# Performance work log

Measured on AMD Instinct MI355X. Metric: run time of the kernel, lower is better.

The kernel has to match this reference:

```python
import jax, jax.numpy as jnp
import numpy as np

N_TYPES = 4  # global / and / or / leaf node types (indep_weights)


def gcn_layer(x, W_stack, b, edge_src, edge_dst, edge_w, labels, num_nodes):
    # Per-node-type dense projection: compute all 4 projections, then select by label.
    # all4: [4, N, out]
    all4 = jnp.einsum('nd,kdo->kno', x, W_stack)
    support = jnp.take_along_axis(all4, labels[None, :, None].astype(jnp.int32), axis=0)[0]  # [N, out]
    # Sparse adjacency propagation: out[dst] += w * support[src]  (torch.spmm equivalent)
    msgs = support[edge_src] * edge_w[:, None]  # [E, out]
    agg = jax.ops.segment_sum(msgs, edge_dst, num_segments=num_nodes)
    return agg + b


def setup_inputs() -> dict:
    key = jax.random.key(0)
    ks = jax.random.split(key, 12)
    N, E = 50000, 1600000
    nfeat, nhid, nclass = 256, 256, 64
    x = jax.random.normal(ks[0], (N, nfeat), dtype=jnp.float32)
    edge_src = jax.random.randint(ks[1], (E,), 0, N, dtype=jnp.int32)
    edge_dst = jax.random.randint(ks[2], (E,), 0, N, dtype=jnp.int32)
    edge_w = jax.random.uniform(ks[3], (E,), dtype=jnp.float32)
    labels = jax.random.randint(ks[4], (N,), 0, N_TYPES, dtype=jnp.int32)
    def winit(k, fi, fo):
        s = 1.0 / np.sqrt(fo)
        return jax.random.uniform(k, (N_TYPES, fi, fo), minval=-s, maxval=s, dtype=jnp.float32)
    def binit(k, fo):
        s = 1.0 / np.sqrt(fo)
        return jax.random.uniform(k, (fo,), minval=-s, maxval=s, dtype=jnp.float32)
    return {
        'x': x, 'edge_src': edge_src, 'edge_dst': edge_dst, 'edge_w': edge_w, 'labels': labels,
        'W1': winit(ks[5], nfeat, nhid), 'b1': binit(ks[6], nhid),
        'W2': winit(ks[7], nhid, nhid), 'b2': binit(ks[8], nhid),
        'W3': winit(ks[9], nhid, nclass), 'b3': binit(ks[10], nclass),
    }


def reference(x, edge_src, edge_dst, edge_w, labels, W1, b1, W2, b2, W3, b3):
    N = x.shape[0]
    h = jax.nn.relu(gcn_layer(x, W1, b1, edge_src, edge_dst, edge_w, labels, N))
    # F.dropout with p=0 (module default) is identity
    h = jax.nn.relu(gcn_layer(h, W2, b2, edge_src, edge_dst, edge_w, labels, N))
    out = gcn_layer(h, W3, b3, edge_src, edge_dst, edge_w, labels, N)
    return out
```

## Files before the change

kernel.cpp:

```cpp
#include <hip/hip_runtime.h>
#include <hip/hip_bf16.h>

#define NT 4
#define FEAT 256
#define OUT3 64

typedef __bf16 bf16x8 __attribute__((ext_vector_type(8)));
typedef float  f32x4  __attribute__((ext_vector_type(4)));

__device__ inline unsigned int f2bf_bits(float f) {
    __hip_bfloat16 h = __float2bfloat16(f);
    unsigned short u;
    __builtin_memcpy(&u, &h, 2);
    return (unsigned int)u;
}
__device__ inline float bfl(unsigned int u) { return __uint_as_float(u << 16); }
__device__ inline float bfh(unsigned int u) { return __uint_as_float(u & 0xffff0000u); }

__global__ void zero_small(int* __restrict__ bcnt, int* __restrict__ lc, int* __restrict__ lcur) {
    int i = threadIdx.x;
    bcnt[i] = 0;
    if (i < NT) { lc[i] = 0; lcur[i] = 0; }
}

__global__ __launch_bounds__(512) void bucket_count(const int* __restrict__ dst,
                                                    const int* __restrict__ labels,
                                                    int* __restrict__ bcnt, int* __restrict__ lc,
                                                    int E, int N) {
    __shared__ int h[256];
    __shared__ int lh[NT];
    int tid = threadIdx.x;
    if (tid < 256) h[tid] = 0;
    if (tid < NT) lh[tid] = 0;
    __syncthreads();
    int base = blockIdx.x * 4096;
#pragma unroll
    for (int k = 0; k < 8; ++k) {
        int e = base + k * 512 + tid;
        if (e < E) atomicAdd(&h[((unsigned)dst[e]) >> 8], 1);
    }
#pragma unroll
    for (int k = 0; k < 8; ++k) {
        int i = base + k * 512 + tid;
        if (i < N) atomicAdd(&lh[labels[i]], 1);
    }
    __syncthreads();
    if (tid < 256) { int v = h[tid]; if (v) atomicAdd(&bcnt[tid], v); }
    if (tid < NT) { int v = lh[tid]; if (v) atomicAdd(&lc[tid], v); }
}

__global__ __launch_bounds__(256) void scan_master(
    const int* __restrict__ bcnt, const int* __restrict__ lc,
    int* __restrict__ boff, int* __restrict__ gcur, int* __restrict__ rowoff,
    int* __restrict__ lstart, int* __restrict__ perm,
    int NB, int N, int E, int permCap) {
    __shared__ int s[256];
    int tid = threadIdx.x;
    int own = (tid < NB) ? bcnt[tid] : 0;
    s[tid] = own;
    __syncthreads();
    for (int d = 1; d < 256; d <<= 1) {
        int v = (tid >= d) ? s[tid - d] : 0;
        __syncthreads();
        s[tid] += v;
        __syncthreads();
    }
    int excl = s[tid] - own;
    if (tid < NB) { boff[tid] = excl; gcur[tid] = excl; }
    if (tid == 0) {
        boff[NB] = E; rowoff[N] = E;
        int run = 0;
        int ls[NT], cnt[NT];
        for (int l = 0; l < NT; ++l) {
            ls[l] = run; cnt[l] = lc[l];
            lstart[l] = run;
            run += (cnt[l] + 63) & ~63;
        }
        for (int l = 0; l < NT; ++l) {
            int end = (l + 1 < NT) ? ls[l + 1] : run;
            for (int i = ls[l] + cnt[l]; i < end; ++i) perm[i] = -1;
        }
        for (int i = run; i < permCap; ++i) perm[i] = -1;
    }
}

__global__ __launch_bounds__(512) void scatter_combined(
    const int* __restrict__ src, const int* __restrict__ dst, const float* __restrict__ w,
    int* __restrict__ gcur, uint2* __restrict__ earr, int E, int nbEB,
    const int* __restrict__ labels, const int* __restrict__ lstart,
    int* __restrict__ lcur, int* __restrict__ perm, int N) {
    int tid = threadIdx.x;
    if ((int)blockIdx.x < nbEB) {
        __shared__ int h[256];
        __shared__ int basearr[256];
        if (tid < 256) h[tid] = 0;
        __syncthreads();
        int base = blockIdx.x * 4096;
        int b[8], rank[8], px[8]; float wv[8];
#pragma unroll
        for (int k = 0; k < 8; ++k) {
            int e = base + k * 512 + tid;
            if (e < E) {
                int d = dst[e];
                b[k] = ((unsigned)d) >> 8;
                px[k] = src[e] | ((d & 255) << 16);
                wv[k] = w[e];
                rank[k] = atomicAdd(&h[b[k]], 1);
            } else b[k] = -1;
        }
        __syncthreads();
        if (tid < 256) { int c = h[tid]; basearr[tid] = c ? atomicAdd(&gcur[tid], c) : 0; }
        __syncthreads();
#pragma unroll
        for (int k = 0; k < 8; ++k) {
            if (b[k] >= 0) {
                int pos = basearr[b[k]] + rank[k];
                earr[pos] = make_uint2((unsigned)px[k], __float_as_uint(wv[k]));
            }
        }
    } else {
        int n = ((int)blockIdx.x - nbEB) * 512 + tid;
        int lab = (n < N) ? labels[n] : -1;
        int lane = tid & 63;
        for (int l = 0; l < NT; ++l) {
            unsigned long long m = __ballot(lab == l);
            if (m == 0ull) continue;
            int leader = __builtin_ctzll(m);
            int base = 0;
            if (lane == leader) base = atomicAdd(&lcur[l], (int)__popcll(m));
            base = __shfl(base, leader, 64);
            if (lab == l) {
                int prefix = (int)__popcll(m & ((1ull << lane) - 1ull));
                perm[lstart[l] + base + prefix] = n;
            }
        }
    }
}

__global__ __launch_bounds__(1024) void bucket_sort(
    const uint2* __restrict__ earr, const int* __restrict__ boff,
    int* __restrict__ rowoff, unsigned int* __restrict__ edata, int N) {
    int b = blockIdx.x;
    int s = boff[b], e = boff[b + 1];
    __shared__ int cnt[256], off[256];
    int tid = threadIdx.x;
    if (tid < 256) cnt[tid] = 0;
    __syncthreads();
    for (int i = s + tid; i < e; i += 1024) atomicAdd(&cnt[(earr[i].x >> 16) & 255], 1);
    __syncthreads();
    if (tid < 256) off[tid] = cnt[tid];
    __syncthreads();
    for (int d = 1; d < 256; d <<= 1) {
        int v = 0;
        if (tid < 256 && tid >= d) v = off[tid - d];
        __syncthreads();
        if (tid < 256) off[tid] += v;
        __syncthreads();
    }
    if (tid < 256) {
        int excl = off[tid] - cnt[tid];
        int node = b * 256 + tid;
        if (node < N) rowoff[node] = s + excl;
        off[tid] = excl;
    }
    __syncthreads();
    for (int i = s + tid; i < e; i += 1024) {
        uint2 r = earr[i];
        int d = (r.x >> 16) & 255;
        int k = atomicAdd(&off[d], 1);
        edata[s + k] = (f2bf_bits(__uint_as_float(r.y)) << 16) | (r.x & 0xffff);
    }
}

__global__ void cast_x(const float* __restrict__ x, unsigned short* __restrict__ xb, int total4) {
    int i = blockIdx.x * 256 + threadIdx.x;
    if (i < total4) {
        const float4* xv = (const float4*)x;
        float4 v = xv[i];
        unsigned int lo = f2bf_bits(v.x) | (f2bf_bits(v.y) << 16);
        unsigned int hi = f2bf_bits(v.z) | (f2bf_bits(v.w) << 16);
        uint2 o; o.x = lo; o.y = hi;
        ((uint2*)xb)[i] = o;
    }
}

__global__ void cast_w_all(const float* __restrict__ W1, const float* __restrict__ W2,
                           const float* __restrict__ W3, unsigned short* __restrict__ W1b,
                           unsigned short* __restrict__ W2b, unsigned short* __restrict__ W3b) {
    const int S = NT * FEAT * FEAT;
    int idx = blockIdx.x * 256 + threadIdx.x;
    const float* W; unsigned short* D; int OUTF; int t;
    if (idx < S)            { W = W1; D = W1b; OUTF = FEAT; t = idx; }
    else if (idx < 2 * S)   { W = W2; D = W2b; OUTF = FEAT; t = idx - S; }
    else if (idx < 2 * S + NT * FEAT * OUT3) { W = W3; D = W3b; OUTF = OUT3; t = idx - 2 * S; }
    else return;
    int n = t % OUTF;
    int r = t / OUTF;
    int j = r & 7, q = (r >> 3) & 3, k0 = (r >> 5) & 7, lab = r >> 8;
    int k = k0 * 32 + q * 8 + j;
    float f = W[((size_t)(lab * FEAT + k)) * OUTF + n];
    D[(((size_t)lab * 8 + k0) * OUTF + n) * 32 + q * 8 + j] = (unsigned short)f2bf_bits(f);
}

__global__ __launch_bounds__(256) void proj256_kernel(
    const unsigned short* __restrict__ xb, const unsigned short* __restrict__ Wswz,
    const int* __restrict__ perm, const int* __restrict__ labels,
    unsigned short* __restrict__ outp) {
    int warp = threadIdx.x >> 6;
    int lane = threadIdx.x & 63;
    int m0 = blockIdx.x * 64;
    int first = perm[m0];
    if (first < 0) return;
    int lab = labels[first];
    int q = lane >> 4, c = lane & 15;
    int n0 = warp * 64;

    const unsigned short* arow[4];
#pragma unroll
    for (int t = 0; t < 4; ++t) {
        int nd = perm[m0 + t * 16 + c];
        arow[t] = xb + (size_t)((nd < 0) ? first : nd) * FEAT;
    }
    const unsigned short* bb = Wswz + (size_t)lab * FEAT * 256 + (size_t)(n0 + c) * 32 + q * 8;

    f32x4 acc[4][4] = {};
#pragma unroll
    for (int k0 = 0; k0 < 8; ++k0) {
        bf16x8 a[4];
#pragma unroll
        for (int t = 0; t < 4; ++t) a[t] = *(const bf16x8*)(arow[t] + k0 * 32 + q * 8);
        const unsigned short* bk = bb + (size_t)k0 * 32 * 256;
#pragma unroll
        for (int u = 0; u < 4; ++u) {
            bf16x8 bfrag = *(const bf16x8*)(bk + u * 512);
#pragma unroll
            for (int t = 0; t < 4; ++t)
                acc[t][u] = __builtin_amdgcn_mfma_f32_16x16x32_bf16(a[t], bfrag, acc[t][u], 0, 0, 0);
        }
    }
    __hip_bfloat16* ob = (__hip_bfloat16*)outp;
#pragma unroll
    for (int t = 0; t < 4; ++t) {
#pragma unroll
        for (int r = 0; r < 4; ++r) {
            int noder = perm[m0 + t * 16 + q * 4 + r];
            if (noder >= 0) {
#pragma unroll
                for (int u = 0; u < 4; ++u)
                    ob[(size_t)noder * 256 + n0 + u * 16 + c] = __float2bfloat16(acc[t][u][r]);
            }
        }
    }
}

__global__ __launch_bounds__(256) void proj64_kernel(
    const unsigned short* __restrict__ xb, const unsigned short* __restrict__ Wswz,
    const int* __restrict__ perm, const int* __restrict__ labels,
    unsigned short* __restrict__ outp) {
    int warp = threadIdx.x >> 6;
    int lane = threadIdx.x & 63;
    int m0 = blockIdx.x * 64;
    int first = perm[m0];
    if (first < 0) return;
    int lab = labels[first];
    int q = lane >> 4, c = lane & 15;
    int mb = m0 + warp * 16;

    int ndc = perm[mb + c];
    const unsigned short* arow = xb + (size_t)((ndc < 0) ? first : ndc) * FEAT;
    const unsigned short* bb = Wswz + (size_t)lab * FEAT * OUT3 + (size_t)c * 32 + q * 8;

    f32x4 acc[4] = {};
#pragma unroll
    for (int k0 = 0; k0 < 8; ++k0) {
        bf16x8 a = *(const bf16x8*)(arow + k0 * 32 + q * 8);
        const unsigned short* bk = bb + (size_t)k0 * 32 * OUT3;
#pragma unroll
        for (int u = 0; u < 4; ++u) {
            bf16x8 bfrag = *(const bf16x8*)(bk + u * 512);
            acc[u] = __builtin_amdgcn_mfma_f32_16x16x32_bf16(a, bfrag, acc[u], 0, 0, 0);
        }
    }
    __hip_bfloat16* ob = (__hip_bfloat16*)outp;
#pragma unroll
    for (int r = 0; r < 4; ++r) {
        int noder = perm[mb + q * 4 + r];
        if (noder >= 0) {
#pragma unroll
            for (int u = 0; u < 4; ++u)
                ob[(size_t)noder * OUT3 + u * 16 + c] = __float2bfloat16(acc[u][r]);
        }
    }
}

__global__ __launch_bounds__(256) void agg256_kernel(
    const uint2* __restrict__ sup, const int* __restrict__ rowoff,
    const unsigned int* __restrict__ edata, const float* __restrict__ bias,
    uint2* __restrict__ outp, int N) {
    int warp = __builtin_amdgcn_readfirstlane((int)(threadIdx.x >> 6));
    int node = (int)blockIdx.x * 4 + warp;
    if (node >= N) return;
    int lane = threadIdx.x & 63;
    int s = __builtin_amdgcn_readfirstlane(rowoff[node]);
    int e = __builtin_amdgcn_readfirstlane(rowoff[node + 1]);
    float a0 = 0.f, a1 = 0.f, a2 = 0.f, a3 = 0.f;
    int j = s;
    for (; j + 8 <= e; j += 8) {
        int ed[8]; uint2 v[8];
#pragma unroll
        for (int u = 0; u < 8; ++u) ed[u] = __builtin_amdgcn_readfirstlane((int)edata[j + u]);
#pragma unroll
        for (int u = 0; u < 8; ++u) v[u] = sup[(size_t)(ed[u] & 0xffff) * 64 + lane];
#pragma unroll
        for (int u = 0; u < 8; ++u) {
            float w = __uint_as_float((unsigned int)ed[u] & 0xffff0000u);
            a0 += w * bfl(v[u].x); a1 += w * bfh(v[u].x);
            a2 += w * bfl(v[u].y); a3 += w * bfh(v[u].y);
        }
    }
    if (j < e) {
        int ed[8]; float wm[8]; uint2 v[8];
#pragma unroll
        for (int u = 0; u < 8; ++u) {
            int jj = j + u;
            int jc = (jj < e) ? jj : e - 1;
            ed[u] = __builtin_amdgcn_readfirstlane((int)edata[jc]);
            wm[u] = (jj < e) ? __uint_as_float((unsigned int)ed[u] & 0xffff0000u) : 0.f;
        }
#pragma unroll
        for (int u = 0; u < 8; ++u) v[u] = sup[(size_t)(ed[u] & 0xffff) * 64 + lane];
#pragma unroll
        for (int u = 0; u < 8; ++u) {
            a0 += wm[u] * bfl(v[u].x); a1 += wm[u] * bfh(v[u].x);
            a2 += wm[u] * bfl(v[u].y); a3 += wm[u] * bfh(v[u].y);
        }
    }
    float4 b = ((const float4*)bias)[lane];
    a0 = fmaxf(a0 + b.x, 0.f);
    a1 = fmaxf(a1 + b.y, 0.f);
    a2 = fmaxf(a2 + b.z, 0.f);
    a3 = fmaxf(a3 + b.w, 0.f);
    unsigned int lo = f2bf_bits(a0) | (f2bf_bits(a1) << 16);
    unsigned int hi = f2bf_bits(a2) | (f2bf_bits(a3) << 16);
    outp[(size_t)node * 64 + lane] = make_uint2(lo, hi);
}

__global__ __launch_bounds__(256) void agg64_kernel(
    const unsigned short* __restrict__ sup, const int* __restrict__ rowoff,
    const unsigned int* __restrict__ edata, const float* __restrict__ bias,
    float* __restrict__ outp, int N) {
    int warp = __builtin_amdgcn_readfirstlane((int)(threadIdx.x >> 6));
    int node = (int)blockIdx.x * 4 + warp;
    if (node >= N) return;
    int lane = threadIdx.x & 63;
    int s = __builtin_amdgcn_readfirstlane(rowoff[node]);
    int e = __builtin_amdgcn_readfirstlane(rowoff[node + 1]);
    float a = 0.f;
    int j = s;
    for (; j + 8 <= e; j += 8) {
        int ed[8]; unsigned short v[8];
#pragma unroll
        for (int u = 0; u < 8; ++u) ed[u] = __builtin_amdgcn_readfirstlane((int)edata[j + u]);
#pragma unroll
        for (int u = 0; u < 8; ++u) v[u] = sup[(size_t)(ed[u] & 0xffff) * 64 + lane];
#pragma unroll
        for (int u = 0; u < 8; ++u)
            a += __uint_as_float((unsigned int)ed[u] & 0xffff0000u) * __uint_as_float((unsigned int)v[u] << 16);
    }
    if (j < e) {
        int ed[8]; float wm[8]; unsigned short v[8];
#pragma unroll
        for (int u = 0; u < 8; ++u) {
            int jj = j + u;
            int jc = (jj < e) ? jj : e - 1;
            ed[u] = __builtin_amdgcn_readfirstlane((int)edata[jc]);
            wm[u] = (jj < e) ? __uint_as_float((unsigned int)ed[u] & 0xffff0000u) : 0.f;
        }
#pragma unroll
        for (int u = 0; u < 8; ++u) v[u] = sup[(size_t)(ed[u] & 0xffff) * 64 + lane];
#pragma unroll
        for (int u = 0; u < 8; ++u)
            a += wm[u] * __uint_as_float((unsigned int)v[u] << 16);
    }
    a += bias[lane];
    outp[(size_t)node * 64 + lane] = a;
}

extern "C" void kernel_launch(void* const* d_in, const int* in_sizes, int n_in,
                              void* d_out, int out_size, void* d_ws, size_t ws_size,
                              hipStream_t stream) {
    const float* x        = (const float*)d_in[0];
    const int*   edge_src = (const int*)d_in[1];
    const int*   edge_dst = (const int*)d_in[2];
    const float* edge_w   = (const float*)d_in[3];
    const int*   labels   = (const int*)d_in[4];
    const float* W1 = (const float*)d_in[5];
    const float* b1 = (const float*)d_in[6];
    const float* W2 = (const float*)d_in[7];
    const float* b2 = (const float*)d_in[8];
    const float* W3 = (const float*)d_in[9];
    const float* b3 = (const float*)d_in[10];

    const int N = in_sizes[0] / FEAT;
    const int E = in_sizes[1];
    const int NB = (N + 255) >> 8;
    const int G64 = (N + NT * 64 + 63) / 64;
    const int permCap = G64 * 64;

    char* p = (char*)d_ws;
    auto alloc = [&](size_t bytes) -> char* {
        char* r = p;
        p += (bytes + 255) & ~(size_t)255;
        return r;
    };
    unsigned short* bufA = (unsigned short*)alloc((size_t)N * FEAT * 2);
    unsigned short* bufB = (unsigned short*)alloc((size_t)N * FEAT * 2);
    unsigned short* W1b  = (unsigned short*)alloc((size_t)NT * FEAT * FEAT * 2);
    unsigned short* W2b  = (unsigned short*)alloc((size_t)NT * FEAT * FEAT * 2);
    unsigned short* W3b  = (unsigned short*)alloc((size_t)NT * FEAT * OUT3 * 2);
    int*          rowoff = (int*)alloc((size_t)(N + 1) * 4);
    unsigned int* edata  = (unsigned int*)alloc((size_t)E * 4);
    int*          perm   = (int*)alloc((size_t)permCap * 4);
    int*          bcnt   = (int*)alloc(256 * 4);
    int*          boff   = (int*)alloc(257 * 4);
    int*          gcur   = (int*)alloc(256 * 4);
    int*          lc     = (int*)alloc(64);
    int*          lcur   = (int*)alloc(64);
    int*          lstart = (int*)alloc(64);
    uint2* earr = (uint2*)bufA;

    const int nbEB = (E + 4095) / 4096;
    const int nbN  = (N + 511) / 512;

    zero_small<<<1, 256, 0, stream>>>(bcnt, lc, lcur);
    bucket_count<<<nbEB, 512, 0, stream>>>(edge_dst, labels, bcnt, lc, E, N);
    scan_master<<<1, 256, 0, stream>>>(bcnt, lc, boff, gcur, rowoff, lstart, perm, NB, N, E, permCap);
    scatter_combined<<<nbEB + nbN, 512, 0, stream>>>(edge_src, edge_dst, edge_w, gcur, earr, E, nbEB,
                                                     labels, lstart, lcur, perm, N);
    bucket_sort<<<NB, 1024, 0, stream>>>(earr, boff, rowoff, edata, N);

    cast_x<<<((N * FEAT / 4) + 255) / 256, 256, 0, stream>>>(x, bufA, N * FEAT / 4);
    {
        int totalW = 2 * NT * FEAT * FEAT + NT * FEAT * OUT3;
        cast_w_all<<<(totalW + 255) / 256, 256, 0, stream>>>(W1, W2, W3, W1b, W2b, W3b);
    }

    proj256_kernel<<<G64, 256, 0, stream>>>(bufA, W1b, perm, labels, bufB);
    agg256_kernel<<<(N + 3) / 4, 256, 0, stream>>>((const uint2*)bufB, rowoff, edata, b1, (uint2*)bufA, N);
    proj256_kernel<<<G64, 256, 0, stream>>>(bufA, W2b, perm, labels, bufB);
    agg256_kernel<<<(N + 3) / 4, 256, 0, stream>>>((const uint2*)bufB, rowoff, edata, b2, (uint2*)bufA, N);
    proj64_kernel<<<G64, 256, 0, stream>>>(bufA, W3b, perm, labels, bufB);
    agg64_kernel<<<(N + 3) / 4, 256, 0, stream>>>(bufB, rowoff, edata, b3, (float*)d_out, N);
}
```

Measured before the change: 510.0 us.

## Store activations in label-sorted slot order with permuted feature columns

Replaces the node-to-slot gather/scatter in the projection kernels with a label-sorted slot layout. Activations live contiguously per label group, edges reference slot indices directly, and feature columns are stored in an MFMA-output-friendly permuted order. Weights and biases are pre-permuted to match, so projection epilogues become packed vector stores and the first-layer input is scattered once during the cast. Aggregation now writes to the node's slot and loads edge words per lane instead of via readfirstlane. This adds an iperm lookup in the edge scatter and more complex index bookkeeping, with the risk of subtle permutation mismatches.

```diff
diff --git a/kernel.cpp b/kernel.cpp
--- a/kernel.cpp
+++ b/kernel.cpp
@@ -16,6 +16,10 @@
 }
 __device__ inline float bfl(unsigned int u) { return __uint_as_float(u << 16); }
 __device__ inline float bfh(unsigned int u) { return __uint_as_float(u & 0xffff0000u); }
+__device__ __host__ inline int nat_of(int p) {
+    int lo = p & 63;
+    return (p & ~63) | (((lo & 3) << 4) | (lo >> 2));
+}
 
 __global__ void zero_small(int* __restrict__ bcnt, int* __restrict__ lc, int* __restrict__ lcur) {
     int i = threadIdx.x;
@@ -23,10 +27,10 @@
     if (i < NT) { lc[i] = 0; lcur[i] = 0; }
 }
 
-__global__ __launch_bounds__(512) void bucket_count(const int* __restrict__ dst,
-                                                    const int* __restrict__ labels,
-                                                    int* __restrict__ bcnt, int* __restrict__ lc,
-                                                    int E, int N) {
+__global__ __launch_bounds__(512) void pass_a(const int* __restrict__ dst,
+                                              const int* __restrict__ labels,
+                                              int* __restrict__ bcnt, int* __restrict__ lc,
+                                              int E, int N) {
     __shared__ int h[256];
     __shared__ int lh[NT];
     int tid = threadIdx.x;
@@ -52,8 +56,7 @@
 __global__ __launch_bounds__(256) void scan_master(
     const int* __restrict__ bcnt, const int* __restrict__ lc,
     int* __restrict__ boff, int* __restrict__ gcur, int* __restrict__ rowoff,
-    int* __restrict__ lstart, int* __restrict__ perm,
-    int NB, int N, int E, int permCap) {
+    int* __restrict__ lstart, int NB, int N, int E) {
     __shared__ int s[256];
     int tid = threadIdx.x;
     int own = (tid < NB) ? bcnt[tid] : 0;
@@ -70,69 +73,61 @@
     if (tid == 0) {
         boff[NB] = E; rowoff[N] = E;
         int run = 0;
-        int ls[NT], cnt[NT];
         for (int l = 0; l < NT; ++l) {
-            ls[l] = run; cnt[l] = lc[l];
             lstart[l] = run;
-            run += (cnt[l] + 63) & ~63;
-        }
-        for (int l = 0; l < NT; ++l) {
-            int end = (l + 1 < NT) ? ls[l + 1] : run;
-            for (int i = ls[l] + cnt[l]; i < end; ++i) perm[i] = -1;
-        }
-        for (int i = run; i < permCap; ++i) perm[i] = -1;
-    }
-}
-
-__global__ __launch_bounds__(512) void scatter_combined(
+            run += (lc[l] + 63) & ~63;
+        }
+    }
+}
+
+__global__ void scatter_nodes(const int* __restrict__ labels, const int* __restrict__ lstart,
+                              int* __restrict__ lcur, int* __restrict__ iperm, int N) {
+    int n = blockIdx.x * 256 + threadIdx.x;
+    int lab = (n < N) ? labels[n] : -1;
+    int lane = threadIdx.x & 63;
+    for (int l = 0; l < NT; ++l) {
+        unsigned long long m = __ballot(lab == l);
+        if (m == 0ull) continue;
+        int leader = __builtin_ctzll(m);
+        int base = 0;
+        if (lane == leader) base = atomicAdd(&lcur[l], (int)__popcll(m));
+        base = __shfl(base, leader, 64);
+        if (lab == l) {
+            int prefix = (int)__popcll(m & ((1ull << lane) - 1ull));
+            iperm[n] = lstart[l] + base + prefix;
+        }
+    }
+}
+
+__global__ __launch_bounds__(512) void scatter_edges(
     const int* __restrict__ src, const int* __restrict__ dst, const float* __restrict__ w,
-    int* __restrict__ gcur, uint2* __restrict__ earr, int E, int nbEB,
-    const int* __restrict__ labels, const int* __restrict__ lstart,
-    int* __restrict__ lcur, int* __restrict__ perm, int N) {
+    const int* __restrict__ iperm, int* __restrict__ gcur, uint2* __restrict__ earr, int E) {
+    __shared__ int h[256];
+    __shared__ int basearr[256];
     int tid = threadIdx.x;
-    if ((int)blockIdx.x < nbEB) {
-        __shared__ int h[256];
-        __shared__ int basearr[256];
-        if (tid < 256) h[tid] = 0;
-        __syncthreads();
-        int base = blockIdx.x * 4096;
-        int b[8], rank[8], px[8]; float wv[8];
-#pragma unroll
-        for (int k = 0; k < 8; ++k) {
-            int e = base + k * 512 + tid;
-            if (e < E) {
-                int d = dst[e];
-                b[k] = ((unsigned)d) >> 8;
-                px[k] = src[e] | ((d & 255) << 16);
-                wv[k] = w[e];
-                rank[k] = atomicAdd(&h[b[k]], 1);
-            } else b[k] = -1;
-        }
-        __syncthreads();
-        if (tid < 256) { int c = h[tid]; basearr[tid] = c ? atomicAdd(&gcur[tid], c) : 0; }
-        __syncthreads();
-#pragma unroll
-        for (int k = 0; k < 8; ++k) {
-            if (b[k] >= 0) {
-                int pos = basearr[b[k]] + rank[k];
-                earr[pos] = make_uint2((unsigned)px[k], __float_as_uint(wv[k]));
-            }
-        }
-    } else {
-        int n = ((int)blockIdx.x - nbEB) * 512 + tid;
-        int lab = (n < N) ? labels[n] : -1;
-        int lane = tid & 63;
-        for (int l = 0; l < NT; ++l) {
-            unsigned long long m = __ballot(lab == l);
-            if (m == 0ull) continue;
-            int leader = __builtin_ctzll(m);
-            int base = 0;
-            if (lane == leader) base = atomicAdd(&lcur[l], (int)__popcll(m));
-            base = __shfl(base, leader, 64);
-            if (lab == l) {
-                int prefix = (int)__popcll(m & ((1ull << lane) - 1ull));
-                perm[lstart[l] + base + prefix] = n;
-            }
+    if (tid < 256) h[tid] = 0;
+    __syncthreads();
+    int base = blockIdx.x * 4096;
+    int b[8], rank[8], px[8]; float wv[8];
+#pragma unroll
+    for (int k = 0; k < 8; ++k) {
+        int e = base + k * 512 + tid;
+        if (e < E) {
+            int d = dst[e];
+            b[k] = ((unsigned)d) >> 8;
+            px[k] = iperm[src[e]] | ((d & 255) << 16);
+            wv[k] = w[e];
+            rank[k] = atomicAdd(&h[b[k]], 1);
+        } else b[k] = -1;
+    }
+    __syncthreads();
+    if (tid < 256) { int c = h[tid]; basearr[tid] = c ? atomicAdd(&gcur[tid], c) : 0; }
+    __syncthreads();
+#pragma unroll
+    for (int k = 0; k < 8; ++k) {
+        if (b[k] >= 0) {
+            int pos = basearr[b[k]] + rank[k];
+            earr[pos] = make_uint2((unsigned)px[k], __float_as_uint(wv[k]));
         }
     }
 }
@@ -172,55 +167,56 @@
     }
 }
 
-__global__ void cast_x(const float* __restrict__ x, unsigned short* __restrict__ xb, int total4) {
+__global__ void cast_x(const float* __restrict__ x, const int* __restrict__ iperm,
+                       unsigned short* __restrict__ xb, int total4) {
     int i = blockIdx.x * 256 + threadIdx.x;
     if (i < total4) {
-        const float4* xv = (const float4*)x;
-        float4 v = xv[i];
+        float4 v = ((const float4*)x)[i];
         unsigned int lo = f2bf_bits(v.x) | (f2bf_bits(v.y) << 16);
         unsigned int hi = f2bf_bits(v.z) | (f2bf_bits(v.w) << 16);
-        uint2 o; o.x = lo; o.y = hi;
-        ((uint2*)xb)[i] = o;
+        int slot = iperm[i >> 6];
+        ((uint2*)xb)[(size_t)slot * 64 + (i & 63)] = make_uint2(lo, hi);
     }
 }
 
 __global__ void cast_w_all(const float* __restrict__ W1, const float* __restrict__ W2,
-                           const float* __restrict__ W3, unsigned short* __restrict__ W1b,
-                           unsigned short* __restrict__ W2b, unsigned short* __restrict__ W3b) {
+                           const float* __restrict__ W3, const float* __restrict__ b1,
+                           const float* __restrict__ b2,
+                           unsigned short* __restrict__ W1b, unsigned short* __restrict__ W2b,
+                           unsigned short* __restrict__ W3b, float* __restrict__ biasPerm) {
     const int S = NT * FEAT * FEAT;
+    const int S3 = NT * FEAT * OUT3;
     int idx = blockIdx.x * 256 + threadIdx.x;
-    const float* W; unsigned short* D; int OUTF; int t;
-    if (idx < S)            { W = W1; D = W1b; OUTF = FEAT; t = idx; }
-    else if (idx < 2 * S)   { W = W2; D = W2b; OUTF = FEAT; t = idx - S; }
-    else if (idx < 2 * S + NT * FEAT * OUT3) { W = W3; D = W3b; OUTF = OUT3; t = idx - 2 * S; }
-    else return;
-    int n = t % OUTF;
-    int r = t / OUTF;
-    int j = r & 7, q = (r >> 3) & 3, k0 = (r >> 5) & 7, lab = r >> 8;
-    int k = k0 * 32 + q * 8 + j;
-    float f = W[((size_t)(lab * FEAT + k)) * OUTF + n];
-    D[(((size_t)lab * 8 + k0) * OUTF + n) * 32 + q * 8 + j] = (unsigned short)f2bf_bits(f);
+    if (idx < 2 * S + S3) {
+        const float* W; unsigned short* D; int OUTF; int t; bool remap;
+        if (idx < S)          { W = W1; D = W1b; OUTF = FEAT; t = idx;         remap = false; }
+        else if (idx < 2 * S) { W = W2; D = W2b; OUTF = FEAT; t = idx - S;     remap = true; }
+        else                  { W = W3; D = W3b; OUTF = OUT3; t = idx - 2 * S; remap = true; }
+        int n = t % OUTF;
+        int r = t / OUTF;
+        int j = r & 7, q = (r >> 3) & 3, k0 = (r >> 5) & 7, lab = r >> 8;
+        int k_slot = k0 * 32 + q * 8 + j;
+        int k_src = remap ? nat_of(k_slot) : k_slot;
+        float f = W[((size_t)(lab * FEAT + k_src)) * OUTF + n];
+        D[(((size_t)lab * 8 + k0) * OUTF + n) * 32 + q * 8 + j] = (unsigned short)f2bf_bits(f);
+    } else {
+        int p = idx - (2 * S + S3);
+        if (p < 256) biasPerm[p] = b1[nat_of(p)];
+        else if (p < 512) biasPerm[p] = b2[nat_of(p - 256) ];
+    }
 }
 
 __global__ __launch_bounds__(256) void proj256_kernel(
     const unsigned short* __restrict__ xb, const unsigned short* __restrict__ Wswz,
-    const int* __restrict__ perm, const int* __restrict__ labels,
-    unsigned short* __restrict__ outp) {
+    const int* __restrict__ lstart, unsigned short* __restrict__ outp) {
     int warp = threadIdx.x >> 6;
     int lane = threadIdx.x & 63;
     int m0 = blockIdx.x * 64;
-    int first = perm[m0];
-    if (first < 0) return;
-    int lab = labels[first];
+    int lab = (m0 >= lstart[1]) + (m0 >= lstart[2]) + (m0 >= lstart[3]);
     int q = lane >> 4, c = lane & 15;
     int n0 = warp * 64;
 
-    const unsigned short* arow[4];
-#pragma unroll
-    for (int t = 0; t < 4; ++t) {
-        int nd = perm[m0 + t * 16 + c];
-        arow[t] = xb + (size_t)((nd < 0) ? first : nd) * FEAT;
-    }
+    const unsigned short* abase = xb + (size_t)m0 * FEAT + (size_t)c * FEAT + q * 8;
     const unsigned short* bb = Wswz + (size_t)lab * FEAT * 256 + (size_t)(n0 + c) * 32 + q * 8;
 
     f32x4 acc[4][4] = {};
@@ -228,7 +224,7 @@
     for (int k0 = 0; k0 < 8; ++k0) {
         bf16x8 a[4];
 #pragma unroll
-        for (int t = 0; t < 4; ++t) a[t] = *(const bf16x8*)(arow[t] + k0 * 32 + q * 8);
+        for (int t = 0; t < 4; ++t) a[t] = *(const bf16x8*)(abase + (size_t)t * 16 * FEAT + k0 * 32);
         const unsigned short* bk = bb + (size_t)k0 * 32 * 256;
 #pragma unroll
         for (int u = 0; u < 4; ++u) {
@@ -238,42 +234,36 @@
                 acc[t][u] = __builtin_amdgcn_mfma_f32_16x16x32_bf16(a[t], bfrag, acc[t][u], 0, 0, 0);
         }
     }
-    __hip_bfloat16* ob = (__hip_bfloat16*)outp;
+    uint2* ov = (uint2*)outp;
 #pragma unroll
     for (int t = 0; t < 4; ++t) {
 #pragma unroll
         for (int r = 0; r < 4; ++r) {
-            int noder = perm[m0 + t * 16 + q * 4 + r];
-            if (noder >= 0) {
-#pragma unroll
-                for (int u = 0; u < 4; ++u)
-                    ob[(size_t)noder * 256 + n0 + u * 16 + c] = __float2bfloat16(acc[t][u][r]);
-            }
+            int row = m0 + t * 16 + q * 4 + r;
+            unsigned int lo = f2bf_bits(acc[t][0][r]) | (f2bf_bits(acc[t][1][r]) << 16);
+            unsigned int hi = f2bf_bits(acc[t][2][r]) | (f2bf_bits(acc[t][3][r]) << 16);
+            ov[(size_t)row * 64 + (n0 >> 2) + c] = make_uint2(lo, hi);
         }
     }
 }
 
 __global__ __launch_bounds__(256) void proj64_kernel(
     const unsigned short* __restrict__ xb, const unsigned short* __restrict__ Wswz,
-    const int* __restrict__ perm, const int* __restrict__ labels,
-    unsigned short* __restrict__ outp) {
+    const int* __restrict__ lstart, unsigned short* __restrict__ outp) {
     int warp = threadIdx.x >> 6;
     int lane = threadIdx.x & 63;
     int m0 = blockIdx.x * 64;
-    int first = perm[m0];
-    if (first < 0) return;
-    int lab = labels[first];
+    int lab = (m0 >= lstart[1]) + (m0 >= lstart[2]) + (m0 >= lstart[3]);
     int q = lane >> 4, c = lane & 15;
     int mb = m0 + warp * 16;
 
-    int ndc = perm[mb + c];
-    const unsigned short* arow = xb + (size_t)((ndc < 0) ? first : ndc) * FEAT;
+    const unsigned short* arow = xb + (size_t)(mb + c) * FEAT + q * 8;
     const unsigned short* bb = Wswz + (size_t)lab * FEAT * OUT3 + (size_t)c * 32 + q * 8;
 
     f32x4 acc[4] = {};
 #pragma unroll
     for (int k0 = 0; k0 < 8; ++k0) {
-        bf16x8 a = *(const bf16x8*)(arow + k0 * 32 + q * 8);
+        bf16x8 a = *(const bf16x8*)(arow + k0 * 32);
         const unsigned short* bk = bb + (size_t)k0 * 32 * OUT3;
 #pragma unroll
         for (int u = 0; u < 4; ++u) {
@@ -281,51 +271,50 @@
             acc[u] = __builtin_amdgcn_mfma_f32_16x16x32_bf16(a, bfrag, acc[u], 0, 0, 0);
         }
     }
-    __hip_bfloat16* ob = (__hip_bfloat16*)outp;
+    uint2* ov = (uint2*)outp;
 #pragma unroll
     for (int r = 0; r < 4; ++r) {
-        int noder = perm[mb + q * 4 + r];
-        if (noder >= 0) {
-#pragma unroll
-            for (int u = 0; u < 4; ++u)
-                ob[(size_t)noder * OUT3 + u * 16 + c] = __float2bfloat16(acc[u][r]);
-        }
+        int row = mb + q * 4 + r;
+        unsigned int lo = f2bf_bits(acc[0][r]) | (f2bf_bits(acc[1][r]) << 16);
+        unsigned int hi = f2bf_bits(acc[2][r]) | (f2bf_bits(acc[3][r]) << 16);
+        ov[(size_t)row * 16 + c] = make_uint2(lo, hi);
     }
 }
 
 __global__ __launch_bounds__(256) void agg256_kernel(
     const uint2* __restrict__ sup, const int* __restrict__ rowoff,
-    const unsigned int* __restrict__ edata, const float* __restrict__ bias,
-    uint2* __restrict__ outp, int N) {
+    const unsigned int* __restrict__ edata, const int* __restrict__ iperm,
+    const float* __restrict__ biasPerm, uint2* __restrict__ outp, int N) {
     int warp = __builtin_amdgcn_readfirstlane((int)(threadIdx.x >> 6));
     int node = (int)blockIdx.x * 4 + warp;
     if (node >= N) return;
     int lane = threadIdx.x & 63;
     int s = __builtin_amdgcn_readfirstlane(rowoff[node]);
     int e = __builtin_amdgcn_readfirstlane(rowoff[node + 1]);
+    int slot = __builtin_amdgcn_readfirstlane(iperm[node]);
     float a0 = 0.f, a1 = 0.f, a2 = 0.f, a3 = 0.f;
     int j = s;
     for (; j + 8 <= e; j += 8) {
-        int ed[8]; uint2 v[8];
-#pragma unroll
-        for (int u = 0; u < 8; ++u) ed[u] = __builtin_amdgcn_readfirstlane((int)edata[j + u]);
+        unsigned int ed[8]; uint2 v[8];
+#pragma unroll
+        for (int u = 0; u < 8; ++u) ed[u] = edata[j + u];
 #pragma unroll
         for (int u = 0; u < 8; ++u) v[u] = sup[(size_t)(ed[u] & 0xffff) * 64 + lane];
 #pragma unroll
         for (int u = 0; u < 8; ++u) {
-            float w = __uint_as_float((unsigned int)ed[u] & 0xffff0000u);
+            float w = __uint_as_float(ed[u] & 0xffff0000u);
             a0 += w * bfl(v[u].x); a1 += w * bfh(v[u].x);
             a2 += w * bfl(v[u].y); a3 += w * bfh(v[u].y);
         }
     }
     if (j < e) {
-        int ed[8]; float wm[8]; uint2 v[8];
+        unsigned int ed[8]; float wm[8]; uint2 v[8];
 #pragma unroll
         for (int u = 0; u < 8; ++u) {
             int jj = j + u;
             int jc = (jj < e) ? jj : e - 1;
-            ed[u] = __builtin_amdgcn_readfirstlane((int)edata[jc]);
-            wm[u] = (jj < e) ? __uint_as_float((unsigned int)ed[u] & 0xffff0000u) : 0.f;
+            ed[u] = edata[jc];
+            wm[u] = (jj < e) ? __uint_as_float(ed[u] & 0xffff0000u) : 0.f;
         }
 #pragma unroll
         for (int u = 0; u < 8; ++u) v[u] = sup[(size_t)(ed[u] & 0xffff) * 64 + lane];
@@ -335,19 +324,19 @@
             a2 += wm[u] * bfl(v[u].y); a3 += wm[u] * bfh(v[u].y);
         }
     }
-    float4 b = ((const float4*)bias)[lane];
+    float4 b = ((const float4*)biasPerm)[lane];
     a0 = fmaxf(a0 + b.x, 0.f);
     a1 = fmaxf(a1 + b.y, 0.f);
     a2 = fmaxf(a2 + b.z, 0.f);
     a3 = fmaxf(a3 + b.w, 0.f);
     unsigned int lo = f2bf_bits(a0) | (f2bf_bits(a1) << 16);
     unsigned int hi = f2bf_bits(a2) | (f2bf_bits(a3) << 16);
-    outp[(size_t)node * 64 + lane] = make_uint2(lo, hi);
+    outp[(size_t)slot * 64 + lane] = make_uint2(lo, hi);
 }
 
 __global__ __launch_bounds__(256) void agg64_kernel(
     const unsigned short* __restrict__ sup, const int* __restrict__ rowoff,
-    const unsigned int* __restrict__ edata, const float* __restrict__ bias,
+    const unsigned int* __restrict__ edata, const float* __restrict__ b3,
     float* __restrict__ outp, int N) {
     int warp = __builtin_amdgcn_readfirstlane((int)(threadIdx.x >> 6));
     int node = (int)blockIdx.x * 4 + warp;
@@ -358,23 +347,23 @@
     float a = 0.f;
     int j = s;
     for (; j + 8 <= e; j += 8) {
-        int ed[8]; unsigned short v[8];
-#pragma unroll
-        for (int u = 0; u < 8; ++u) ed[u] = __builtin_amdgcn_readfirstlane((int)edata[j + u]);
+        unsigned int ed[8]; unsigned short v[8];
+#pragma unroll
+        for (int u = 0; u < 8; ++u) ed[u] = edata[j + u];
 #pragma unroll
         for (int u = 0; u < 8; ++u) v[u] = sup[(size_t)(ed[u] & 0xffff) * 64 + lane];
 #pragma unroll
         for (int u = 0; u < 8; ++u)
-            a += __uint_as_float((unsigned int)ed[u] & 0xffff0000u) * __uint_as_float((unsigned int)v[u] << 16);
+            a += __uint_as_float(ed[u] & 0xffff0000u) * __uint_as_float((unsigned int)v[u] << 16);
     }
     if (j < e) {
-        int ed[8]; float wm[8]; unsigned short v[8];
+        unsigned int ed[8]; float wm[8]; unsigned short v[8];
 #pragma unroll
         for (int u = 0; u < 8; ++u) {
             int jj = j + u;
             int jc = (jj < e) ? jj : e - 1;
-            ed[u] = __builtin_amdgcn_readfirstlane((int)edata[jc]);
-            wm[u] = (jj < e) ? __uint_as_float((unsigned int)ed[u] & 0xffff0000u) : 0.f;
+            ed[u] = edata[jc];
+            wm[u] = (jj < e) ? __uint_as_float(ed[u] & 0xffff0000u) : 0.f;
         }
 #pragma unroll
         for (int u = 0; u < 8; ++u) v[u] = sup[(size_t)(ed[u] & 0xffff) * 64 + lane];
@@ -382,8 +371,8 @@
         for (int u = 0; u < 8; ++u)
             a += wm[u] * __uint_as_float((unsigned int)v[u] << 16);
     }
-    a += bias[lane];
-    outp[(size_t)node * 64 + lane] = a;
+    int natp = (((lane & 3) << 4) | (lane >> 2));
+    outp[(size_t)node * 64 + natp] = a + b3[natp];
 }
 
 extern "C" void kernel_launch(void* const* d_in, const int* in_sizes, int n_in,
@@ -405,7 +394,7 @@
     const int E = in_sizes[1];
     const int NB = (N + 255) >> 8;
     const int G64 = (N + NT * 64 + 63) / 64;
-    const int permCap = G64 * 64;
+    const int slotCap = G64 * 64;
 
     char* p = (char*)d_ws;
     auto alloc = [&](size_t bytes) -> char* {
@@ -413,14 +402,15 @@
         p += (bytes + 255) & ~(size_t)255;
         return r;
     };
-    unsigned short* bufA = (unsigned short*)alloc((size_t)N * FEAT * 2);
-    unsigned short* bufB = (unsigned short*)alloc((size_t)N * FEAT * 2);
+    unsigned short* bufA = (unsigned short*)alloc((size_t)slotCap * FEAT * 2);
+    unsigned short* bufB = (unsigned short*)alloc((size_t)slotCap * FEAT * 2);
     unsigned short* W1b  = (unsigned short*)alloc((size_t)NT * FEAT * FEAT * 2);
     unsigned short* W2b  = (unsigned short*)alloc((size_t)NT * FEAT * FEAT * 2);
     unsigned short* W3b  = (unsigned short*)alloc((size_t)NT * FEAT * OUT3 * 2);
+    float*        biasPerm = (float*)alloc(512 * 4);
     int*          rowoff = (int*)alloc((size_t)(N + 1) * 4);
     unsigned int* edata  = (unsigned int*)alloc((size_t)E * 4);
-    int*          perm   = (int*)alloc((size_t)permCap * 4);
+    int*          iperm  = (int*)alloc((size_t)N * 4);
     int*          bcnt   = (int*)alloc(256 * 4);
     int*          boff   = (int*)alloc(257 * 4);
     int*          gcur   = (int*)alloc(256 * 4);
@@ -430,25 +420,24 @@
     uint2* earr = (uint2*)bufA;
 
     const int nbEB = (E + 4095) / 4096;
-    const int nbN  = (N + 511) / 512;
 
     zero_small<<<1, 256, 0, stream>>>(bcnt, lc, lcur);
-    bucket_count<<<nbEB, 512, 0, stream>>>(edge_dst, labels, bcnt, lc, E, N);
-    scan_master<<<1, 256, 0, stream>>>(bcnt, lc, boff, gcur, rowoff, lstart, perm, NB, N, E, permCap);
-    scatter_combined<<<nbEB + nbN, 512, 0, stream>>>(edge_src, edge_dst, edge_w, gcur, earr, E, nbEB,
-                                                     labels, lstart, lcur, perm, N);
+    pass_a<<<nbEB, 512, 0, stream>>>(edge_dst, labels, bcnt, lc, E, N);
+    scan_master<<<1, 256, 0, stream>>>(bcnt, lc, boff, gcur, rowoff, lstart, NB, N, E);
+    scatter_nodes<<<(N + 255) / 256, 256, 0, stream>>>(labels, lstart, lcur, iperm, N);
+    scatter_edges<<<nbEB, 512, 0, stream>>>(edge_src, edge_dst, edge_w, iperm, gcur, earr, E);
     bucket_sort<<<NB, 1024, 0, stream>>>(earr, boff, rowoff, edata, N);
 
-    cast_x<<<((N * FEAT / 4) + 255) / 256, 256, 0, stream>>>(x, bufA, N * FEAT / 4);
+    cast_x<<<((N * 64) + 255) / 256, 256, 0, stream>>>(x, iperm, bufA, N * 64);
     {
-        int totalW = 2 * NT * FEAT * FEAT + NT * FEAT * OUT3;
-        cast_w_all<<<(totalW + 255) / 256, 256, 0, stream>>>(W1, W2, W3, W1b, W2b, W3b);
-    }
-
-    proj256_kernel<<<G64, 256, 0, stream>>>(bufA, W1b, perm, labels, bufB);
-    agg256_kernel<<<(N + 3) / 4, 256, 0, stream>>>((const uint2*)bufB, rowoff, edata, b1, (uint2*)bufA, N);
-    proj256_kernel<<<G64, 256, 0, stream>>>(bufA, W2b, perm, labels, bufB);
-    agg256_kernel<<<(N + 3) / 4, 256, 0, stream>>>((const uint2*)bufB, rowoff, edata, b2, (uint2*)bufA, N);
-    proj64_kernel<<<G64, 256, 0, stream>>>(bufA, W3b, perm, labels, bufB);
+        int total = 2 * NT * FEAT * FEAT + NT * FEAT * OUT3 + 512;
+        cast_w_all<<<(total + 255) / 256, 256, 0, stream>>>(W1, W2, W3, b1, b2, W1b, W2b, W3b, biasPerm);
+    }
+
+    proj256_kernel<<<G64, 256, 0, stream>>>(bufA, W1b, lstart, bufB);
+    agg256_kernel<<<(N + 3) / 4, 256, 0, stream>>>((const uint2*)bufB, rowoff, edata, iperm, biasPerm, (uint2*)bufA, N);
+    proj256_kernel<<<G64, 256, 0, stream>>>(bufA, W2b, lstart, bufB);
+    agg256_kernel<<<(N + 3) / 4, 256, 0, stream>>>((const uint2*)bufB, rowoff, edata, iperm, biasPerm + 256, (uint2*)bufA, N);
+    proj64_kernel<<<G64, 256, 0, stream>>>(bufA, W3b, lstart, bufB);
     agg64_kernel<<<(N + 3) / 4, 256, 0, stream>>>(bufB, rowoff, edata, b3, (float*)d_out, N);
 }
```

After: 506.2 us. Within noise of the previous version (-0.7%).
